# Performance work log

Measured on AMD Instinct MI355X. Metric: run time of the kernel, lower is better.

The kernel has to match this reference:

```python
import jax, jax.numpy as jnp
import numpy as np

D_MODEL = 768
EXPAND = 2
D_STATE = 128
HEADDIM = 64
D_CONV = 4
D_INNER = EXPAND * D_MODEL            # 1536
NHEADS = D_INNER // HEADDIM           # 24
CONV_DIM = D_INNER + 2 * D_STATE      # 1792
D_IN_PROJ = 2 * D_INNER + 2 * D_STATE + NHEADS  # 3352
EPS = 1e-5
BATCH, SEQLEN = 2, 2048


def silu(v):
    return v * jax.nn.sigmoid(v)


def mamba2(x, in_w, conv_w, conv_b, dt_bias, A_log, Dp, norm_w, out_w):
    # x: (b, l, d_model)
    b, l, _ = x.shape
    zxbcdt = x @ in_w.T                              # (b, l, d_in_proj)
    z = zxbcdt[..., :D_INNER]
    xBC = zxbcdt[..., D_INNER:D_INNER + CONV_DIM]
    dt = jax.nn.softplus(zxbcdt[..., D_INNER + CONV_DIM:] + dt_bias)  # (b, l, h)
    # causal depthwise conv1d, kernel D_CONV, left padding D_CONV-1
    pad = jnp.pad(xBC, ((0, 0), (D_CONV - 1, 0), (0, 0)))
    conv = conv_b
    for k in range(D_CONV):
        conv = conv + pad[:, k:k + l, :] * conv_w[:, k]
    xBC = silu(conv)
    xh = xBC[..., :D_INNER].reshape(b, l, NHEADS, HEADDIM)   # (b,l,h,p)
    Bm = xBC[..., D_INNER:D_INNER + D_STATE]                 # (b,l,n) ngroups=1
    Cm = xBC[..., D_INNER + D_STATE:]                        # (b,l,n)
    A = -jnp.exp(A_log)                                      # (h,)
    dA = jnp.exp(dt * A)                                     # (b,l,h)

    def step(h, inp):
        dA_t, dt_t, x_t, B_t, C_t = inp
        # h: (b, h, p, n)
        h = h * dA_t[:, :, None, None] + (dt_t[:, :, None] * x_t)[..., None] * B_t[:, None, None, :]
        y = jnp.einsum('bhpn,bn->bhp', h, C_t)
        return h, y

    h0 = jnp.zeros((b, NHEADS, HEADDIM, D_STATE), x.dtype)
    xs = (dA.transpose(1, 0, 2), dt.transpose(1, 0, 2), xh.transpose(1, 0, 2, 3),
          Bm.transpose(1, 0, 2), Cm.transpose(1, 0, 2))
    _, ys = jax.lax.scan(step, h0, xs)                       # (l,b,h,p)
    y = ys.transpose(1, 0, 2, 3) + Dp[None, None, :, None] * xh
    y = y.reshape(b, l, D_INNER)
    # RMSNormGated (norm_before_gate=False): rmsnorm(y * silu(z)) * weight
    y = y * silu(z)
    y = y * jax.lax.rsqrt(jnp.mean(jnp.square(y), axis=-1, keepdims=True) + EPS) * norm_w
    return y @ out_w.T


def setup_inputs() -> dict:
    key = jax.random.key(0)
    ks = jax.random.split(key, 9)
    s = 0.02
    return {
        'x': jax.random.normal(ks[0], (BATCH, SEQLEN, D_MODEL), jnp.float32),
        'in_proj_w': jax.random.normal(ks[1], (2, D_IN_PROJ, D_MODEL), jnp.float32) * s,
        'conv_w': jax.random.normal(ks[2], (2, CONV_DIM, D_CONV), jnp.float32) * 0.2,
        'conv_b': jax.random.normal(ks[3], (2, CONV_DIM), jnp.float32) * s,
        'dt_bias': jax.random.normal(ks[4], (2, NHEADS), jnp.float32) * 0.1,
        'A_log': jnp.log(jax.random.uniform(ks[5], (2, NHEADS), jnp.float32, 1.0, 16.0)),
        'D': jax.random.normal(ks[6], (2, NHEADS), jnp.float32) * 0.5 + 1.0,
        'norm_w': jnp.ones((2, D_INNER), jnp.float32),
        'out_proj_w': jax.random.normal(ks[7], (2, D_MODEL, D_INNER), jnp.float32) * s,
    }


def reference(x, in_proj_w, conv_w, conv_b, dt_bias, A_log, D, norm_w, out_proj_w):
    h_fwd = mamba2(x, in_proj_w[0], conv_w[0], conv_b[0], dt_bias[0], A_log[0], D[0], norm_w[0], out_proj_w[0])
    x_rev = jnp.flip(x, axis=1)
    h_bwd_rev = mamba2(x_rev, in_proj_w[1], conv_w[1], conv_b[1], dt_bias[1], A_log[1], D[1], norm_w[1], out_proj_w[1])
    return h_fwd + jnp.flip(h_bwd_rev, axis=1)
```

## Files before the change

kernel.cpp:

```cpp
#include <hip/hip_runtime.h>
#include <hip/hip_bf16.h>

typedef __attribute__((ext_vector_type(8))) short short8;
typedef __attribute__((ext_vector_type(4))) short bfx4;
typedef __attribute__((ext_vector_type(4))) float floatx4;

#define SEQ     2048
#define DMODEL  768
#define DINNER  1536
#define DSTATE  128
#define NH      24
#define CONVDIM 1792
#define NPROJ   3352
#define QCH     64
#define NCH     (SEQ / QCH)

__device__ inline float bf2f(short s) {
    return __uint_as_float(((unsigned)(unsigned short)s) << 16);
}
__device__ inline short f2bf(float f) {
    __hip_bfloat16 h = __float2bfloat16(f);
    return *reinterpret_cast<short*>(&h);
}
__device__ inline void gl_lds16(const void* g, void* l) {
    __builtin_amdgcn_global_load_lds((const __attribute__((address_space(1))) unsigned int*)g,
                                     (__attribute__((address_space(3))) unsigned int*)l, 16, 0, 0);
}

__global__ __launch_bounds__(256) void cvt_kernel(const float* __restrict__ src,
                                                  __hip_bfloat16* __restrict__ dst, int n4) {
    int i = blockIdx.x * 256 + threadIdx.x;
    if (i >= n4) return;
    float4 v = *(const float4*)(src + (size_t)i * 4);
    bfx4 o = { f2bf(v.x), f2bf(v.y), f2bf(v.z), f2bf(v.w) };
    *(bfx4*)((short*)dst + (size_t)i * 4) = o;
}

__global__ __launch_bounds__(256) void prep_x_kernel(const float* __restrict__ x,
                                                     __hip_bfloat16* __restrict__ A1) {
    size_t i4 = (size_t)blockIdx.x * 256 + threadIdx.x;
    const size_t total4 = (size_t)2 * 2 * SEQ * DMODEL / 4;
    if (i4 >= total4) return;
    size_t idx = i4 * 4;
    int k = (int)(idx % DMODEL);
    size_t m = idx / DMODEL;
    int dir = (int)(m >> 12);
    int mm  = (int)(m & 4095);
    int b = mm >> 11, t = mm & 2047;
    int ts = dir ? (SEQ - 1 - t) : t;
    float4 v = *(const float4*)(x + ((size_t)(b * SEQ + ts)) * DMODEL + k);
    bfx4 o = { f2bf(v.x), f2bf(v.y), f2bf(v.z), f2bf(v.w) };
    *(bfx4*)((short*)A1 + idx) = o;
}

__global__ __launch_bounds__(256) void gemm_bt(const __hip_bfloat16* __restrict__ Abase, size_t aStride,
                                               const __hip_bfloat16* __restrict__ Bbase, size_t bStride,
                                               float* __restrict__ C,
                                               __hip_bfloat16* __restrict__ Zb,
                                               __hip_bfloat16* __restrict__ Xb,
                                               float* __restrict__ DT,
                                               float* __restrict__ LA,
                                               const float* __restrict__ dtbias,
                                               const float* __restrict__ Alog,
                                               int M, int N, int K, int zdiv, int mode) {
    __shared__ short As[2][128 * 32];
    __shared__ short Bs[2][128 * 32];
    int tid = threadIdx.x;
    int w = tid >> 6, lane = tid & 63;
    int q = lane >> 4, mm = lane & 15;
    int wm = w >> 1, wn = w & 1;
    int m0 = blockIdx.x * 128, n0 = blockIdx.y * 128;
    int z = blockIdx.z;
    int dir = z / zdiv, ks = z - dir * zdiv;
    int kl = K / zdiv;
    int kbeg = ks * kl;
    const short* Ag = (const short*)Abase + (size_t)dir * aStride;
    const short* Bg = (const short*)Bbase + (size_t)dir * bStride;

    int srow = lane >> 2;
    int gch  = (lane & 3) ^ (srow & 3) ^ ((lane >> 4) & 3);

    floatx4 acc[16];
#pragma unroll
    for (int i = 0; i < 16; i++) acc[i] = (floatx4){0.f, 0.f, 0.f, 0.f};

    int niter = kl / 32;
    auto stage = [&](int buf, int k0) {
#pragma unroll
        for (int j = 0; j < 2; j++) {
            int b16 = (w * 2 + j) * 16;
            int ar = m0 + b16 + srow;
            gl_lds16(Ag + (size_t)ar * K + kbeg + k0 + gch * 8, (char*)&As[buf][0] + b16 * 64);
            int br = n0 + b16 + srow; if (br > N - 1) br = N - 1;
            gl_lds16(Bg + (size_t)br * K + kbeg + k0 + gch * 8, (char*)&Bs[buf][0] + b16 * 64);
        }
    };
    stage(0, 0);
    int p = q ^ (mm & 3) ^ ((mm >> 2) & 3);
    for (int it = 0; it < niter; it++) {
        __syncthreads();
        if (it + 1 < niter) stage((it + 1) & 1, (it + 1) * 32);
        const short* Ab = &As[it & 1][0];
        const short* Bb = &Bs[it & 1][0];
        short8 af[4], bfr[4];
#pragma unroll
        for (int mb = 0; mb < 4; mb++)
            af[mb] = *(const short8*)&Ab[(wm * 64 + mb * 16 + mm) * 32 + p * 8];
#pragma unroll
        for (int nb = 0; nb < 4; nb++)
            bfr[nb] = *(const short8*)&Bb[(wn * 64 + nb * 16 + mm) * 32 + p * 8];
#pragma unroll
        for (int mb = 0; mb < 4; mb++)
#pragma unroll
            for (int nb = 0; nb < 4; nb++)
                acc[mb * 4 + nb] = __builtin_amdgcn_mfma_f32_16x16x32_bf16(af[mb], bfr[nb], acc[mb * 4 + nb], 0, 0, 0);
    }

    __hip_bfloat16* Zb2 = Zb + (size_t)dir * 4096 * DINNER;
    __hip_bfloat16* Xb2 = Xb + (size_t)dir * 4096 * CONVDIM;
    float* DT2 = DT + (size_t)dir * 4096 * NH;
    float* LA2 = LA + (size_t)dir * 4096 * NH;
    const float* dtb2 = dtbias + dir * NH;
    const float* Al2  = Alog + dir * NH;

#pragma unroll
    for (int mb = 0; mb < 4; mb++) {
#pragma unroll
        for (int nb = 0; nb < 4; nb++) {
            int col = n0 + wn * 64 + nb * 16 + mm;
            if (col >= N) continue;
#pragma unroll
            for (int r = 0; r < 4; r++) {
                int rr = m0 + wm * 64 + mb * 16 + q * 4 + r;
                float v = acc[mb * 4 + nb][r];
                if (mode == 1) {
                    int orow = rr;
                    if (dir) { int b = rr >> 11, t = rr & 2047; orow = (b << 11) + (2047 - t); }
                    atomicAdd(&C[(size_t)orow * N + col], v);
                } else {
                    if (col < DINNER) {
                        Zb2[(size_t)rr * DINNER + col] = __float2bfloat16(v);
                    } else if (col < DINNER + CONVDIM) {
                        Xb2[(size_t)rr * CONVDIM + (col - DINNER)] = __float2bfloat16(v);
                    } else {
                        int hh = col - (DINNER + CONVDIM);
                        float raw = v + dtb2[hh];
                        float dtv = (raw > 20.f) ? raw : log1pf(__expf(raw));
                        float Av  = -__expf(Al2[hh]);
                        DT2[(size_t)rr * NH + hh] = dtv;
                        LA2[(size_t)rr * NH + hh] = dtv * Av;
                    }
                }
            }
        }
    }
}

__global__ __launch_bounds__(256) void conv_kernel(const __hip_bfloat16* __restrict__ Xb,
                                                   const float* __restrict__ conv_w,
                                                   const float* __restrict__ conv_b,
                                                   __hip_bfloat16* __restrict__ xh,
                                                   __hip_bfloat16* __restrict__ Bm,
                                                   __hip_bfloat16* __restrict__ Cm) {
    int db  = blockIdx.x >> 7;
    int dir = db >> 1;
    int t0  = (blockIdx.x & 127) * 16;
    int c8  = threadIdx.x * 8;
    if (c8 >= CONVDIM) return;

    float wk[4][8], bs[8];
#pragma unroll
    for (int j = 0; j < 8; j++) {
        bs[j] = conv_b[dir * CONVDIM + c8 + j];
#pragma unroll
        for (int k = 0; k < 4; k++) wk[k][j] = conv_w[((size_t)dir * CONVDIM + c8 + j) * 4 + k];
    }

    const short* xrow = (const short*)Xb + (size_t)db * SEQ * CONVDIM + c8;
    short8 win[4];
    const short8 zer = {0, 0, 0, 0, 0, 0, 0, 0};
#pragma unroll
    for (int k = 0; k < 3; k++) {
        int ts = t0 - 3 + k;
        win[k] = (ts >= 0) ? *(const short8*)(xrow + (size_t)ts * CONVDIM) : zer;
    }

    for (int tt = 0; tt < 16; tt++) {
        int t = t0 + tt;
        win[3] = *(const short8*)(xrow + (size_t)t * CONVDIM);
        short8 outv;
#pragma unroll
        for (int j = 0; j < 8; j++) {
            float acc = bs[j];
#pragma unroll
            for (int k = 0; k < 4; k++) acc += wk[k][j] * bf2f(win[k][j]);
            float sv = acc / (1.f + __expf(-acc));
            outv[j] = f2bf(sv);
        }
        if (c8 < DINNER)
            *(short8*)((short*)xh + (size_t)(db * SEQ + t) * DINNER + c8) = outv;
        else if (c8 < DINNER + DSTATE)
            *(short8*)((short*)Bm + (size_t)(db * SEQ + t) * DSTATE + (c8 - DINNER)) = outv;
        else
            *(short8*)((short*)Cm + (size_t)(db * SEQ + t) * DSTATE + (c8 - DINNER - DSTATE)) = outv;
        win[0] = win[1]; win[1] = win[2]; win[2] = win[3];
    }
}

__global__ __launch_bounds__(256) void ssd1_kernel(const __hip_bfloat16* __restrict__ XH,
                                                   const __hip_bfloat16* __restrict__ BMh,
                                                   const float* __restrict__ DT,
                                                   const float* __restrict__ LA,
                                                   short* __restrict__ SS,
                                                   float* __restrict__ CUM) {
    int blk = blockIdx.x;
    int ck = blk & 31;
    int dbh = blk >> 5;
    int hh = dbh % NH, db = dbh / NH;
    int base_row = db * SEQ + ck * QCH;

    __shared__ float cum_s[QCH], dt_s[QCH];
    __shared__ short Xt[64][72];
    __shared__ short Bt[128][72];

    int tid = threadIdx.x;
    int lane = tid & 63, w = tid >> 6;
    int q = lane >> 4, mm = lane & 15;

    if (tid < QCH) {
        float la  = LA[(size_t)(base_row + tid) * NH + hh];
        float dtv = DT[(size_t)(base_row + tid) * NH + hh];
        float cs = la;
#pragma unroll
        for (int d = 1; d < 64; d <<= 1) {
            float u = __shfl_up(cs, d);
            if (tid >= d) cs += u;
        }
        cum_s[tid] = cs;
        dt_s[tid] = dtv;
        CUM[(size_t)dbh * SEQ + ck * QCH + tid] = cs;
    }
    __syncthreads();
    float cumL = cum_s[QCH - 1];

    {
        int s2 = (tid & 31) * 2, pb = tid >> 5;
        float f0 = dt_s[s2]     * __expf(cumL - cum_s[s2]);
        float f1 = dt_s[s2 + 1] * __expf(cumL - cum_s[s2 + 1]);
        const short* r0 = (const short*)XH + (size_t)(base_row + s2) * DINNER + hh * 64 + pb * 8;
        const short* r1 = r0 + DINNER;
        short8 x0 = *(const short8*)r0;
        short8 x1 = *(const short8*)r1;
#pragma unroll
        for (int j = 0; j < 8; j++) {
            unsigned lo = (unsigned short)f2bf(f0 * bf2f(x0[j]));
            unsigned hi = (unsigned short)f2bf(f1 * bf2f(x1[j]));
            *(unsigned*)&Xt[pb * 8 + j][s2] = lo | (hi << 16);
        }
    }
    {
        int s2 = (tid & 31) * 2, nb = tid >> 5;
        const short* r0 = (const short*)BMh + (size_t)(base_row + s2) * DSTATE + nb * 16;
        const short* r1 = r0 + DSTATE;
        short8 b0a = *(const short8*)r0,  b0b = *(const short8*)(r0 + 8);
        short8 b1a = *(const short8*)r1,  b1b = *(const short8*)(r1 + 8);
#pragma unroll
        for (int j = 0; j < 8; j++) {
            *(unsigned*)&Bt[nb * 16 + j][s2] =
                (unsigned)(unsigned short)b0a[j] | ((unsigned)(unsigned short)b1a[j] << 16);
            *(unsigned*)&Bt[nb * 16 + 8 + j][s2] =
                (unsigned)(unsigned short)b0b[j] | ((unsigned)(unsigned short)b1b[j] << 16);
        }
    }
    __syncthreads();

    floatx4 acc[8];
#pragma unroll
    for (int i = 0; i < 8; i++) acc[i] = (floatx4){0.f, 0.f, 0.f, 0.f};
#pragma unroll
    for (int kk = 0; kk < 2; kk++) {
        short8 a = *(const short8*)&Xt[w * 16 + mm][kk * 32 + q * 8];
#pragma unroll
        for (int cb = 0; cb < 8; cb++) {
            short8 b = *(const short8*)&Bt[cb * 16 + mm][kk * 32 + q * 8];
            acc[cb] = __builtin_amdgcn_mfma_f32_16x16x32_bf16(a, b, acc[cb], 0, 0, 0);
        }
    }
    short* Sp = SS + (size_t)blk * 8192;
#pragma unroll
    for (int cb = 0; cb < 8; cb++)
#pragma unroll
        for (int r = 0; r < 4; r++)
            Sp[(w * 16 + q * 4 + r) * DSTATE + cb * 16 + mm] = f2bf(acc[cb][r]);
}

__global__ __launch_bounds__(256) void ssd2_kernel(const short* __restrict__ SS,
                                                   const float* __restrict__ CUM,
                                                   short* __restrict__ Hprev) {
    int blk = blockIdx.x;
    int dbh = blk >> 2, part = blk & 3;
    int off = part * 2048 + threadIdx.x * 8;
    size_t base = (size_t)dbh * NCH * 8192 + off;
    float h[8];
#pragma unroll
    for (int j = 0; j < 8; j++) h[j] = 0.f;
    for (int c = 0; c < NCH; c++) {
        float W = __expf(CUM[(size_t)dbh * SEQ + c * QCH + QCH - 1]);
        size_t p = base + (size_t)c * 8192;
        short8 s = *(const short8*)(SS + p);
        short8 o;
#pragma unroll
        for (int j = 0; j < 8; j++) o[j] = f2bf(h[j]);
        *(short8*)(Hprev + p) = o;
#pragma unroll
        for (int j = 0; j < 8; j++) h[j] = fmaf(h[j], W, bf2f(s[j]));
    }
}

__global__ __launch_bounds__(256) void ssd3_kernel(const __hip_bfloat16* __restrict__ XH,
                                                   const __hip_bfloat16* __restrict__ BMh,
                                                   const __hip_bfloat16* __restrict__ CMh,
                                                   const float* __restrict__ DT,
                                                   const float* __restrict__ CUM,
                                                   const short* __restrict__ Hprev,
                                                   __hip_bfloat16* __restrict__ Yb) {
    int blk = blockIdx.x;
    int ck = blk & 31;
    int dbh = blk >> 5;
    int hh = dbh % NH, db = dbh / NH;
    int base_row = db * SEQ + ck * QCH;

    __shared__ float cum_s[QCH], dt_s[QCH];
    __shared__ short Ct[64][136];
    __shared__ short G[64][72];
    __shared__ short Xt[64][72];

    int tid = threadIdx.x;
    int lane = tid & 63, w = tid >> 6;
    int q = lane >> 4, mm = lane & 15;

    if (tid < QCH) {
        cum_s[tid] = CUM[(size_t)dbh * SEQ + ck * QCH + tid];
        dt_s[tid]  = DT[(size_t)(base_row + tid) * NH + hh];
    }

    const short* Cg = (const short*)CMh + (size_t)base_row * DSTATE;
    const short* Bg = (const short*)BMh + (size_t)base_row * DSTATE;
    floatx4 P[4];
#pragma unroll
    for (int i = 0; i < 4; i++) P[i] = (floatx4){0.f, 0.f, 0.f, 0.f};
#pragma unroll
    for (int kk = 0; kk < 4; kk++) {
        short8 a = *(const short8*)(Cg + (size_t)(w * 16 + mm) * DSTATE + kk * 32 + q * 8);
#pragma unroll
        for (int cb = 0; cb < 4; cb++) {
            short8 b = *(const short8*)(Bg + (size_t)(cb * 16 + mm) * DSTATE + kk * 32 + q * 8);
            P[cb] = __builtin_amdgcn_mfma_f32_16x16x32_bf16(a, b, P[cb], 0, 0, 0);
        }
    }
    __syncthreads();

    {
        int t = tid & 63, nb4 = tid >> 6;
        float wt = __expf(cum_s[t]);
        const short* src = Cg + (size_t)t * DSTATE + nb4 * 32;
#pragma unroll
        for (int u = 0; u < 2; u++) {
            short8 v = *(const short8*)(src + u * 16);
            short8 v2 = *(const short8*)(src + u * 16 + 8);
#pragma unroll
            for (int j = 0; j < 4; j++) {
                unsigned lo = (unsigned short)f2bf(wt * bf2f(v[2 * j]));
                unsigned hi = (unsigned short)f2bf(wt * bf2f(v[2 * j + 1]));
                *(unsigned*)&Ct[t][nb4 * 32 + u * 16 + 2 * j] = lo | (hi << 16);
                lo = (unsigned short)f2bf(wt * bf2f(v2[2 * j]));
                hi = (unsigned short)f2bf(wt * bf2f(v2[2 * j + 1]));
                *(unsigned*)&Ct[t][nb4 * 32 + u * 16 + 8 + 2 * j] = lo | (hi << 16);
            }
        }
    }
    {
        int s2 = (tid & 31) * 2, pb = tid >> 5;
        const short* r0 = (const short*)XH + (size_t)(base_row + s2) * DINNER + hh * 64 + pb * 8;
        const short* r1 = r0 + DINNER;
        short8 x0 = *(const short8*)r0;
        short8 x1 = *(const short8*)r1;
#pragma unroll
        for (int j = 0; j < 8; j++) {
            *(unsigned*)&Xt[pb * 8 + j][s2] =
                (unsigned)(unsigned short)x0[j] | ((unsigned)(unsigned short)x1[j] << 16);
        }
    }
#pragma unroll
    for (int cb = 0; cb < 4; cb++) {
#pragma unroll
        for (int r = 0; r < 4; r++) {
            int t = w * 16 + q * 4 + r;
            int s = cb * 16 + mm;
            float g = (s <= t) ? P[cb][r] * __expf(cum_s[t] - cum_s[s]) * dt_s[s] : 0.f;
            G[t][s] = f2bf(g);
        }
    }
    __syncthreads();

    floatx4 Y[4];
#pragma unroll
    for (int i = 0; i < 4; i++) Y[i] = (floatx4){0.f, 0.f, 0.f, 0.f};
#pragma unroll
    for (int kk = 0; kk < 2; kk++) {
        short8 a = *(const short8*)&G[w * 16 + mm][kk * 32 + q * 8];
#pragma unroll
        for (int cb = 0; cb < 4; cb++) {
            short8 b = *(const short8*)&Xt[cb * 16 + mm][kk * 32 + q * 8];
            Y[cb] = __builtin_amdgcn_mfma_f32_16x16x32_bf16(a, b, Y[cb], 0, 0, 0);
        }
    }
    const short* Hc = Hprev + (size_t)blk * 8192;
#pragma unroll
    for (int kk = 0; kk < 4; kk++) {
        short8 a = *(const short8*)&Ct[w * 16 + mm][kk * 32 + q * 8];
#pragma unroll
        for (int cb = 0; cb < 4; cb++) {
            short8 b = *(const short8*)(Hc + (size_t)(cb * 16 + mm) * DSTATE + kk * 32 + q * 8);
            Y[cb] = __builtin_amdgcn_mfma_f32_16x16x32_bf16(a, b, Y[cb], 0, 0, 0);
        }
    }
#pragma unroll
    for (int cb = 0; cb < 4; cb++)
#pragma unroll
        for (int r = 0; r < 4; r++)
            Yb[(size_t)(base_row + w * 16 + q * 4 + r) * DINNER + hh * 64 + cb * 16 + mm] =
                __float2bfloat16(Y[cb][r]);
}

__global__ __launch_bounds__(192) void gate_kernel(const __hip_bfloat16* __restrict__ Yb,
                                                   const __hip_bfloat16* __restrict__ xh,
                                                   const __hip_bfloat16* __restrict__ Zb,
                                                   const float* __restrict__ Dp,
                                                   const float* __restrict__ norm_w,
                                                   __hip_bfloat16* __restrict__ A2) {
    int row = blockIdx.x;
    int dir = row >> 12;
    int c8 = threadIdx.x * 8;
    int hd = c8 >> 6;
    const short* yr = (const short*)Yb + (size_t)row * DINNER + c8;
    const short* xr = (const short*)xh + (size_t)row * DINNER + c8;
    const short* zr = (const short*)Zb + (size_t)row * DINNER + c8;

    short8 y8 = *(const short8*)yr;
    short8 x8 = *(const short8*)xr;
    short8 z8 = *(const short8*)zr;
    float Dv = Dp[dir * NH + hd];

    float vals[8];
    float ss = 0.f;
#pragma unroll
    for (int j = 0; j < 8; j++) {
        float v = bf2f(y8[j]) + Dv * bf2f(x8[j]);
        float z = bf2f(z8[j]);
        v *= z / (1.f + __expf(-z));
        vals[j] = v;
        ss += v * v;
    }
#pragma unroll
    for (int off = 32; off; off >>= 1) ss += __shfl_down(ss, off);
    __shared__ float ls[3];
    if ((threadIdx.x & 63) == 0) ls[threadIdx.x >> 6] = ss;
    __syncthreads();
    float tot = ls[0] + ls[1] + ls[2];
    float scale = rsqrtf(tot / (float)DINNER + 1e-5f);

    const float* nw = norm_w + dir * DINNER + c8;
    short8 o;
#pragma unroll
    for (int j = 0; j < 8; j++) o[j] = f2bf(vals[j] * scale * nw[j]);
    *(short8*)((short*)A2 + (size_t)row * DINNER + c8) = o;
}

extern "C" void kernel_launch(void* const* d_in, const int* in_sizes, int n_in,
                              void* d_out, int out_size, void* d_ws, size_t ws_size,
                              hipStream_t stream) {
    const float* x        = (const float*)d_in[0];
    const float* in_w     = (const float*)d_in[1];
    const float* conv_w   = (const float*)d_in[2];
    const float* conv_b   = (const float*)d_in[3];
    const float* dt_bias  = (const float*)d_in[4];
    const float* A_log    = (const float*)d_in[5];
    const float* Dp       = (const float*)d_in[6];
    const float* norm_w   = (const float*)d_in[7];
    const float* out_w    = (const float*)d_in[8];
    float* out = (float*)d_out;

    const size_t szW2 = (size_t)2 * DMODEL * DINNER * 2;
    const size_t szZ  = (size_t)8192 * DINNER * 2;
    const size_t szXH = (size_t)8192 * DINNER * 2;
    const size_t szBM = (size_t)8192 * DSTATE * 2;
    const size_t szCM = szBM;
    const size_t szDT = (size_t)8192 * NH * 4;
    const size_t szLA = szDT;
    const size_t szA1 = (size_t)8192 * DMODEL * 2;
    const size_t szW1 = (size_t)2 * NPROJ * DMODEL * 2;
    const size_t szXB = (size_t)8192 * CONVDIM * 2;
    const size_t szYb = (size_t)8192 * DINNER * 2;
    const size_t szSS = (size_t)96 * NCH * 8192 * 2;
    const size_t szRa = szA1 + szW1 + szXB;
    size_t szR = szRa;
    if (szR < szYb) szR = szYb;
    if (szR < szSS) szR = szSS;
    const size_t szHp = szSS;
    const size_t szCU = (size_t)96 * SEQ * 4;

    char* ws = (char*)d_ws;
    size_t off = 0;
    auto alloc = [&](size_t bytes) { char* p = ws + off; off += (bytes + 255) & ~(size_t)255; return p; };

    __hip_bfloat16* W2 = (__hip_bfloat16*)alloc(szW2);
    __hip_bfloat16* Z  = (__hip_bfloat16*)alloc(szZ);
    __hip_bfloat16* XH = (__hip_bfloat16*)alloc(szXH);
    __hip_bfloat16* BM = (__hip_bfloat16*)alloc(szBM);
    __hip_bfloat16* CM = (__hip_bfloat16*)alloc(szCM);
    float* DT = (float*)alloc(szDT);
    float* LA = (float*)alloc(szLA);
    char*  R  = (char*)alloc(szR);
    __hip_bfloat16* A1  = (__hip_bfloat16*)R;
    __hip_bfloat16* W1  = (__hip_bfloat16*)(R + szA1);
    __hip_bfloat16* XBC = (__hip_bfloat16*)(R + szA1 + szW1);
    short* SS = (short*)R;
    __hip_bfloat16* Yb = (__hip_bfloat16*)R;

    short* Hp = (short*)alloc(szHp);
    float* CU = (float*)alloc(szCU);
    if (off > ws_size) return;

    int n1 = 2 * NPROJ * DMODEL / 4;
    cvt_kernel<<<(n1 + 255) / 256, 256, 0, stream>>>(in_w, W1, n1);
    int n2 = 2 * DMODEL * DINNER / 4;
    cvt_kernel<<<(n2 + 255) / 256, 256, 0, stream>>>(out_w, W2, n2);
    int n3 = 2 * 4096 * DMODEL / 4;
    prep_x_kernel<<<(n3 + 255) / 256, 256, 0, stream>>>(x, A1);

    {
        dim3 grid(4096 / 128, (NPROJ + 127) / 128, 2);
        gemm_bt<<<grid, 256, 0, stream>>>(A1, (size_t)4096 * DMODEL,
                                          W1, (size_t)NPROJ * DMODEL,
                                          nullptr, Z, XBC, DT, LA, dt_bias, A_log,
                                          4096, NPROJ, DMODEL, 1, 2);
    }

    conv_kernel<<<4 * 128, 256, 0, stream>>>(XBC, conv_w, conv_b, XH, BM, CM);

    ssd1_kernel<<<4 * NH * NCH, 256, 0, stream>>>(XH, BM, DT, LA, SS, CU);
    ssd2_kernel<<<4 * NH * 4, 256, 0, stream>>>(SS, CU, Hp);
    ssd3_kernel<<<4 * NH * NCH, 256, 0, stream>>>(XH, BM, CM, DT, CU, Hp, Yb);

    gate_kernel<<<2 * 4096, 192, 0, stream>>>(Yb, XH, Z, Dp, norm_w, Z);

    hipMemsetAsync(out, 0, (size_t)4096 * DMODEL * 4, stream);
    {
        dim3 grid(4096 / 128, DMODEL / 128, 4);
        gemm_bt<<<grid, 256, 0, stream>>>(Z, (size_t)4096 * DINNER,
                                          W2, (size_t)DMODEL * DINNER,
                                          out, nullptr, nullptr, nullptr, nullptr, nullptr, nullptr,
                                          4096, DMODEL, DINNER, 2, 1);
    }
}
```

Before: 389.1 us.

## Fold sequence flip into GEMM loads and change LDS tile swizzle layout

```diff
diff --git a/kernel.cpp b/kernel.cpp
--- a/kernel.cpp
+++ b/kernel.cpp
@@ -36,23 +36,6 @@
     *(bfx4*)((short*)dst + (size_t)i * 4) = o;
 }
 
-__global__ __launch_bounds__(256) void prep_x_kernel(const float* __restrict__ x,
-                                                     __hip_bfloat16* __restrict__ A1) {
-    size_t i4 = (size_t)blockIdx.x * 256 + threadIdx.x;
-    const size_t total4 = (size_t)2 * 2 * SEQ * DMODEL / 4;
-    if (i4 >= total4) return;
-    size_t idx = i4 * 4;
-    int k = (int)(idx % DMODEL);
-    size_t m = idx / DMODEL;
-    int dir = (int)(m >> 12);
-    int mm  = (int)(m & 4095);
-    int b = mm >> 11, t = mm & 2047;
-    int ts = dir ? (SEQ - 1 - t) : t;
-    float4 v = *(const float4*)(x + ((size_t)(b * SEQ + ts)) * DMODEL + k);
-    bfx4 o = { f2bf(v.x), f2bf(v.y), f2bf(v.z), f2bf(v.w) };
-    *(bfx4*)((short*)A1 + idx) = o;
-}
-
 __global__ __launch_bounds__(256) void gemm_bt(const __hip_bfloat16* __restrict__ Abase, size_t aStride,
                                                const __hip_bfloat16* __restrict__ Bbase, size_t bStride,
                                                float* __restrict__ C,
@@ -62,9 +45,9 @@
                                                float* __restrict__ LA,
                                                const float* __restrict__ dtbias,
                                                const float* __restrict__ Alog,
-                                               int M, int N, int K, int zdiv, int mode) {
-    __shared__ short As[2][128 * 32];
-    __shared__ short Bs[2][128 * 32];
+                                               int M, int N, int K, int zdiv, int mode, int flipA) {
+    __shared__ short As[2][64 * 64];
+    __shared__ short Bs[2][64 * 64];
     int tid = threadIdx.x;
     int w = tid >> 6, lane = tid & 63;
     int q = lane >> 4, mm = lane & 15;
@@ -76,9 +59,25 @@
     int kbeg = ks * kl;
     const short* Ag = (const short*)Abase + (size_t)dir * aStride;
     const short* Bg = (const short*)Bbase + (size_t)dir * bStride;
-
-    int srow = lane >> 2;
-    int gch  = (lane & 3) ^ (srow & 3) ^ ((lane >> 4) & 3);
+    int fA = flipA && dir;
+
+    size_t aoff[2], boff[2];
+    int ldso[2];
+#pragma unroll
+    for (int j = 0; j < 2; j++) {
+        int widx = w * 2 + j;
+        int ln = widx * 8 + (lane >> 3);
+        int s  = lane & 7;
+        int c  = s ^ (ln & 7);
+        int row = (c < 4) ? ln : ln + 64;
+        int ch  = (c < 4) ? c : (c ^ 4);
+        int ar = m0 + row;
+        if (fA) { int bb = ar >> 11, tt = ar & 2047; ar = (bb << 11) + (2047 - tt); }
+        aoff[j] = (size_t)ar * K + ch * 8;
+        int br = n0 + row; if (br > N - 1) br = N - 1;
+        boff[j] = (size_t)br * K + ch * 8;
+        ldso[j] = widx * 1024;
+    }
 
     floatx4 acc[16];
 #pragma unroll
@@ -88,15 +87,13 @@
     auto stage = [&](int buf, int k0) {
 #pragma unroll
         for (int j = 0; j < 2; j++) {
-            int b16 = (w * 2 + j) * 16;
-            int ar = m0 + b16 + srow;
-            gl_lds16(Ag + (size_t)ar * K + kbeg + k0 + gch * 8, (char*)&As[buf][0] + b16 * 64);
-            int br = n0 + b16 + srow; if (br > N - 1) br = N - 1;
-            gl_lds16(Bg + (size_t)br * K + kbeg + k0 + gch * 8, (char*)&Bs[buf][0] + b16 * 64);
+            gl_lds16(Ag + aoff[j] + kbeg + k0, (char*)&As[buf][0] + ldso[j]);
+            gl_lds16(Bg + boff[j] + kbeg + k0, (char*)&Bs[buf][0] + ldso[j]);
         }
     };
     stage(0, 0);
-    int p = q ^ (mm & 3) ^ ((mm >> 2) & 3);
+    int slotA = (q ^ (mm & 7) ^ (wm << 2)) * 8;
+    int slotB = (q ^ (mm & 7) ^ (wn << 2)) * 8;
     for (int it = 0; it < niter; it++) {
         __syncthreads();
         if (it + 1 < niter) stage((it + 1) & 1, (it + 1) * 32);
@@ -105,10 +102,10 @@
         short8 af[4], bfr[4];
 #pragma unroll
         for (int mb = 0; mb < 4; mb++)
-            af[mb] = *(const short8*)&Ab[(wm * 64 + mb * 16 + mm) * 32 + p * 8];
+            af[mb] = *(const short8*)&Ab[(mb * 16 + mm) * 64 + slotA];
 #pragma unroll
         for (int nb = 0; nb < 4; nb++)
-            bfr[nb] = *(const short8*)&Bb[(wn * 64 + nb * 16 + mm) * 32 + p * 8];
+            bfr[nb] = *(const short8*)&Bb[(nb * 16 + mm) * 64 + slotB];
 #pragma unroll
         for (int mb = 0; mb < 4; mb++)
 #pragma unroll
@@ -498,7 +495,7 @@
     const size_t szCM = szBM;
     const size_t szDT = (size_t)8192 * NH * 4;
     const size_t szLA = szDT;
-    const size_t szA1 = (size_t)8192 * DMODEL * 2;
+    const size_t szA1 = (size_t)4096 * DMODEL * 2;
     const size_t szW1 = (size_t)2 * NPROJ * DMODEL * 2;
     const size_t szXB = (size_t)8192 * CONVDIM * 2;
     const size_t szYb = (size_t)8192 * DINNER * 2;
@@ -536,15 +533,15 @@
     cvt_kernel<<<(n1 + 255) / 256, 256, 0, stream>>>(in_w, W1, n1);
     int n2 = 2 * DMODEL * DINNER / 4;
     cvt_kernel<<<(n2 + 255) / 256, 256, 0, stream>>>(out_w, W2, n2);
-    int n3 = 2 * 4096 * DMODEL / 4;
-    prep_x_kernel<<<(n3 + 255) / 256, 256, 0, stream>>>(x, A1);
+    int n3 = 4096 * DMODEL / 4;
+    cvt_kernel<<<(n3 + 255) / 256, 256, 0, stream>>>(x, A1, n3);
 
     {
         dim3 grid(4096 / 128, (NPROJ + 127) / 128, 2);
-        gemm_bt<<<grid, 256, 0, stream>>>(A1, (size_t)4096 * DMODEL,
+        gemm_bt<<<grid, 256, 0, stream>>>(A1, 0,
                                           W1, (size_t)NPROJ * DMODEL,
                                           nullptr, Z, XBC, DT, LA, dt_bias, A_log,
-                                          4096, NPROJ, DMODEL, 1, 2);
+                                          4096, NPROJ, DMODEL, 1, 2, 1);
     }
 
     conv_kernel<<<4 * 128, 256, 0, stream>>>(XBC, conv_w, conv_b, XH, BM, CM);
@@ -561,6 +558,6 @@
         gemm_bt<<<grid, 256, 0, stream>>>(Z, (size_t)4096 * DINNER,
                                           W2, (size_t)DMODEL * DINNER,
                                           out, nullptr, nullptr, nullptr, nullptr, nullptr, nullptr,
-                                          4096, DMODEL, DINNER, 2, 1);
-    }
-}
+                                          4096, DMODEL, DINNER, 2, 1, 0);
+    }
+}
```

Result: no change. 385.9 us, median of 2 (-0.8%).
